# Kernel tuning notes

Measured on AMD Instinct MI355X. Metric: run time of the kernel, lower is better.

## Reference

```python
import jax, jax.numpy as jnp
import numpy as np

B, T, F, H, FC1, NC = 16384, 56, 56, 20, 128, 2


def setup_inputs() -> dict:
    key = jax.random.key(0)
    ks = jax.random.split(key, 12)
    s_in = 1.0 / np.sqrt(H)  # PyTorch GRU init scale
    d = {
        'x': jax.random.normal(ks[0], (B, T, F), jnp.float32),
        'W_ih0': jax.random.uniform(ks[1], (3 * H, F), jnp.float32, -s_in, s_in),
        'W_hh0': jax.random.uniform(ks[2], (3 * H, H), jnp.float32, -s_in, s_in),
        'b_ih0': jax.random.uniform(ks[3], (3 * H,), jnp.float32, -s_in, s_in),
        'b_hh0': jax.random.uniform(ks[4], (3 * H,), jnp.float32, -s_in, s_in),
        'W_ih1': jax.random.uniform(ks[5], (3 * H, H), jnp.float32, -s_in, s_in),
        'W_hh1': jax.random.uniform(ks[6], (3 * H, H), jnp.float32, -s_in, s_in),
        'b_ih1': jax.random.uniform(ks[7], (3 * H,), jnp.float32, -s_in, s_in),
        'b_hh1': jax.random.uniform(ks[8], (3 * H,), jnp.float32, -s_in, s_in),
        'W_fc1': jax.random.uniform(ks[9], (FC1, T * H), jnp.float32, -1 / np.sqrt(T * H), 1 / np.sqrt(T * H)),
        'b_fc1': jnp.zeros((FC1,), jnp.float32),
        'W_fc2': jax.random.uniform(ks[10], (NC, FC1), jnp.float32, -1 / np.sqrt(FC1), 1 / np.sqrt(FC1)),
        'b_fc2': jnp.zeros((NC,), jnp.float32),
    }
    return d


def gru_layer(x, W_ih, W_hh, b_ih, b_hh):
    # x: [B, T, Fin] -> output [B, T, H]; PyTorch gate order: r, z, n
    xproj = jnp.einsum('bti,gi->btg', x, W_ih) + b_ih  # [B, T, 3H]

    def step(h, xp):
        gh = h @ W_hh.T + b_hh
        i_r, i_z, i_n = jnp.split(xp, 3, axis=-1)
        h_r, h_z, h_n = jnp.split(gh, 3, axis=-1)
        r = jax.nn.sigmoid(i_r + h_r)
        z = jax.nn.sigmoid(i_z + h_z)
        n = jnp.tanh(i_n + r * h_n)
        h_new = (1.0 - z) * n + z * h
        return h_new, h_new

    h0 = jnp.zeros((x.shape[0], W_hh.shape[1]), x.dtype)
    _, ys = jax.lax.scan(step, h0, jnp.swapaxes(xproj, 0, 1))  # [T, B, H]
    return jnp.swapaxes(ys, 0, 1)


def reference(x, W_ih0, W_hh0, b_ih0, b_hh0, W_ih1, W_hh1, b_ih1, b_hh1,
              W_fc1, b_fc1, W_fc2, b_fc2):
    h1 = gru_layer(x, W_ih0, W_hh0, b_ih0, b_hh0)   # [B, T, H]
    h2 = gru_layer(h1, W_ih1, W_hh1, b_ih1, b_hh1)  # [B, T, H]
    flat = h2.reshape(h2.shape[0], -1)              # [B, T*H]
    y = flat @ W_fc1.T + b_fc1
    y = y @ W_fc2.T + b_fc2
    return y
```

## Files before the change

### kernel.cpp

```cpp
#include <hip/hip_runtime.h>


#define Bsz  16384
#define Tt   56
#define Ff   56
#define Hh   20
#define Gg   60
#define FC1n 128
#define THn  1120
#define BT   (Bsz * Tt)

#define WS_WEFF 0
#define WS_BEFF 2240
#define WS_WT   2242
#define WS_XP   5632
#define WS_NEED_BYTES ((size_t)(WS_XP + (size_t)BT * Gg) * 4)

typedef __attribute__((address_space(1))) const unsigned char gas_uchar;
typedef __attribute__((address_space(3))) unsigned char las_uchar;
typedef __attribute__((ext_vector_type(2))) float f32x2;

__device__ __forceinline__ float rdlane(float v, int l) {
  return __uint_as_float(__builtin_amdgcn_readlane(__float_as_uint(v), l));
}
__device__ __forceinline__ float bperm(int addr, float v) {
  return __uint_as_float(__builtin_amdgcn_ds_bpermute(addr, __float_as_uint(v)));
}
__device__ __forceinline__ float fast_rcp(float x) { return __builtin_amdgcn_rcpf(x); }
__device__ __forceinline__ float sigmoid_fast(float x) { return fast_rcp(1.0f + __expf(-x)); }
__device__ __forceinline__ float tanh_fast(float x) { return 1.0f - 2.0f * fast_rcp(1.0f + __expf(2.0f * x)); }

__device__ __forceinline__ f32x2 mk2(float a, float b) { f32x2 r; r.x = a; r.y = b; return r; }

__device__ __forceinline__ f32x2 pkfma_s(f32x2 hs, f32x2 wv, f32x2 c) {
  f32x2 d;
  asm("v_pk_fma_f32 %0, %1, %2, %3" : "=v"(d) : "s"(hs), "v"(wv), "v"(c));
  return d;
}
__device__ __forceinline__ f32x2 pkfma_v(f32x2 a, f32x2 b, f32x2 c) {
  f32x2 d;
  asm("v_pk_fma_f32 %0, %1, %2, %3" : "=v"(d) : "v"(a), "v"(b), "v"(c));
  return d;
}
__device__ __forceinline__ f32x2 pkfma_w(f32x2 xx, f32x2 w, f32x2 c) {
  f32x2 d;
  asm("v_pk_fma_f32 %0, %1, %2, %3" : "=v"(d) : "v"(xx), "s"(w), "v"(c));
  return d;
}
__device__ __forceinline__ f32x2 pkadd(f32x2 a, f32x2 b) {
  f32x2 d;
  asm("v_pk_add_f32 %0, %1, %2" : "=v"(d) : "v"(a), "v"(b));
  return d;
}

__device__ __forceinline__ void gru_cell(float xg, float hg, int addrR, int addrZ, float& hm) {
  float sg = sigmoid_fast(xg + hg);
  float rr = bperm(addrR, sg);
  float nn = tanh_fast(fmaf(rr, hg, xg));
  float zz = bperm(addrZ, sg);
  hm = fmaf(zz, hm - nn, nn);
}

__global__ void prep_all(const float* __restrict__ Wfc1, const float* __restrict__ bfc1,
                         const float* __restrict__ Wfc2, const float* __restrict__ bfc2,
                         const float* __restrict__ Wih0, float* __restrict__ ws) {
  int i = blockIdx.x * blockDim.x + threadIdx.x;
  if (i < THn) {
    float s0a = 0.f, s1a = 0.f, s0b = 0.f, s1b = 0.f;
    float s0c = 0.f, s1c = 0.f, s0d = 0.f, s1d = 0.f;
#pragma unroll 4
    for (int j = 0; j < FC1n; j += 4) {
      float wa = Wfc1[(j + 0) * THn + i];
      float wb = Wfc1[(j + 1) * THn + i];
      float wc = Wfc1[(j + 2) * THn + i];
      float wd = Wfc1[(j + 3) * THn + i];
      s0a = fmaf(wa, Wfc2[j + 0], s0a); s1a = fmaf(wa, Wfc2[FC1n + j + 0], s1a);
      s0b = fmaf(wb, Wfc2[j + 1], s0b); s1b = fmaf(wb, Wfc2[FC1n + j + 1], s1b);
      s0c = fmaf(wc, Wfc2[j + 2], s0c); s1c = fmaf(wc, Wfc2[FC1n + j + 2], s1c);
      s0d = fmaf(wd, Wfc2[j + 3], s0d); s1d = fmaf(wd, Wfc2[FC1n + j + 3], s1d);
    }
    ws[WS_WEFF + i * 2 + 0] = (s0a + s0b) + (s0c + s0d);
    ws[WS_WEFF + i * 2 + 1] = (s1a + s1b) + (s1c + s1d);
  } else if (i < THn + 2) {
    int c = i - THn;
    float s = bfc2[c];
    for (int j = 0; j < FC1n; ++j) s = fmaf(bfc1[j], Wfc2[c * FC1n + j], s);
    ws[WS_BEFF + c] = s;
  } else if (i < THn + 2 + Ff * Gg) {
    int j = i - (THn + 2);
    int f = j / 60;
    int rem = j % 60;
    int p = rem >> 1, c = rem & 1;
    ws[WS_WT + j] = Wih0[(2 * p + c) * Ff + f];
  }
}

#define PadW 57
__global__ __launch_bounds__(256, 2) void xproj_kernel(
    const float* __restrict__ x, const float* __restrict__ bih0,
    const float* __restrict__ wschunk , float* __restrict__ xp) {
  __shared__ float xs[256 * PadW];
  const int tid = threadIdx.x;
  const size_t blk0 = (size_t)blockIdx.x * 256;

  const float4* xg = (const float4*)(x + blk0 * Ff);
#pragma unroll
  for (int i = 0; i < 14; ++i) {
    int p = i * 256 + tid;
    float4 v = xg[p];
    int r = p / 14, c = p % 14;
    *(float4*)&xs[r * PadW + c * 4] = v;
  }
  __syncthreads();

  f32x2 acc2[30];
  const f32x2* b2 = (const f32x2*)bih0;
#pragma unroll
  for (int p = 0; p < 30; ++p) acc2[p] = b2[p];

  const f32x2* wt2 = (const f32x2*)wschunk;
#pragma unroll 1
  for (int f4 = 0; f4 < 14; ++f4) {
    float4 xv = *(const float4*)&xs[tid * PadW + f4 * 4];
    const f32x2* w0 = wt2 + (size_t)(f4 * 4) * 30;
    {
      f32x2 xx = mk2(xv.x, xv.x);
#pragma unroll
      for (int p = 0; p < 30; ++p) acc2[p] = pkfma_w(xx, w0[p], acc2[p]);
    }
    {
      f32x2 xx = mk2(xv.y, xv.y);
      const f32x2* w = w0 + 30;
#pragma unroll
      for (int p = 0; p < 30; ++p) acc2[p] = pkfma_w(xx, w[p], acc2[p]);
    }
    {
      f32x2 xx = mk2(xv.z, xv.z);
      const f32x2* w = w0 + 60;
#pragma unroll
      for (int p = 0; p < 30; ++p) acc2[p] = pkfma_w(xx, w[p], acc2[p]);
    }
    {
      f32x2 xx = mk2(xv.w, xv.w);
      const f32x2* w = w0 + 90;
#pragma unroll
      for (int p = 0; p < 30; ++p) acc2[p] = pkfma_w(xx, w[p], acc2[p]);
    }
  }
  float4* out = (float4*)(xp + (blk0 + tid) * Gg);
#pragma unroll
  for (int q = 0; q < 15; ++q)
    out[q] = make_float4(acc2[2 * q].x, acc2[2 * q].y, acc2[2 * q + 1].x, acc2[2 * q + 1].y);
}

__global__ __launch_bounds__(256, 4) void gru_scan_xp2(
    const float* __restrict__ xp,
    const float* __restrict__ Whh0, const float* __restrict__ bhh0,
    const float* __restrict__ Wih1, const float* __restrict__ bih1,
    const float* __restrict__ Whh1, const float* __restrict__ bhh1,
    const float* __restrict__ ws, float* __restrict__ y) {
  __shared__ float weff[2 * THn + 2];
  __shared__ __align__(16) float hstage[4][2][64];
  for (int idx = threadIdx.x; idx < 2 * THn + 2; idx += 256) weff[idx] = ws[idx];
  __syncthreads();

  const int lane = threadIdx.x & 63;
  const int wv = threadIdx.x >> 6;
  const int b0 = (blockIdx.x * 4 + wv) * 2;
  const int g = (lane < Gg) ? lane : 0;

  f32x2 whh0p[10], wih1p[10], whh1p[10];
#pragma unroll
  for (int i = 0; i < 10; ++i) whh0p[i] = *(const f32x2*)&Whh0[g * Hh + 2 * i];
#pragma unroll
  for (int i = 0; i < 10; ++i) wih1p[i] = *(const f32x2*)&Wih1[g * Hh + 2 * i];
#pragma unroll
  for (int i = 0; i < 10; ++i) whh1p[i] = *(const f32x2*)&Whh1[g * Hh + 2 * i];

  const f32x2 cb0  = mk2(bhh0[g], 0.f);
  const f32x2 cb1i = mk2(bih1[g], 0.f);
  const f32x2 cb1h = mk2(bhh1[g], 0.f);
  const f32x2 zz2  = mk2(0.f, 0.f);

  float hmA[2] = {0.f, 0.f};
  float hmB[2] = {0.f, 0.f};
  f32x2 hA2[2][10];
#pragma unroll
  for (int e = 0; e < 2; ++e)
#pragma unroll
    for (int i = 0; i < 10; ++i) hA2[e][i] = zz2;

  hstage[wv][0][lane] = 0.f;
  hstage[wv][1][lane] = 0.f;

  float ya[2] = {0.f, 0.f};
  float yb[2] = {0.f, 0.f};

  const int addrR = ((lane >= 40) ? (lane - 40) : lane) * 4;
  const int addrZ = ((lane >= 40) ? (lane - 20) : lane) * 4;
  const int jm = (lane >= 40 && lane < Gg) ? lane - 40 : 0;

  const float* xpb = xp + (size_t)b0 * (Tt * Gg);
  int off[2];
  float xc[2], xn[2];
#pragma unroll
  for (int e = 0; e < 2; ++e) { off[e] = e * (Tt * Gg) + g; xc[e] = xpb[off[e]]; }

#pragma unroll 1
  for (int t = 0; t < Tt; ++t) {
    if (t < Tt - 1) {
#pragma unroll
      for (int e = 0; e < 2; ++e) xn[e] = xpb[off[e] + Gg];
    }
#pragma unroll
    for (int e = 0; e < 2; ++e) {
      f32x2 a = pkfma_s(hA2[e][0], whh0p[0], cb0);
      f32x2 b = pkfma_s(hA2[e][1], whh0p[1], zz2);
#pragma unroll
      for (int i = 2; i < 10; i += 2) {
        a = pkfma_s(hA2[e][i], whh0p[i], a);
        b = pkfma_s(hA2[e][i + 1], whh0p[i + 1], b);
      }
      f32x2 s = pkadd(a, b);
      float hg = s.x + s.y;
      gru_cell(xc[e], hg, addrR, addrZ, hmA[e]);
#pragma unroll
      for (int i = 0; i < 10; ++i)
        hA2[e][i] = mk2(rdlane(hmA[e], 40 + 2 * i), rdlane(hmA[e], 41 + 2 * i));
    }
#pragma unroll
    for (int e = 0; e < 2; ++e) {
      f32x2 ai = pkfma_s(hA2[e][0], wih1p[0], cb1i);
      f32x2 bi = pkfma_s(hA2[e][1], wih1p[1], zz2);
#pragma unroll
      for (int i = 2; i < 10; i += 2) {
        ai = pkfma_s(hA2[e][i], wih1p[i], ai);
        bi = pkfma_s(hA2[e][i + 1], wih1p[i + 1], bi);
      }
      const float4* hb = (const float4*)&hstage[wv][e][40];
      float4 q0 = hb[0], q1 = hb[1], q2 = hb[2], q3 = hb[3], q4 = hb[4];
      f32x2 ah = pkfma_v(mk2(q0.x, q0.y), whh1p[0], cb1h);
      f32x2 bh = pkfma_v(mk2(q0.z, q0.w), whh1p[1], zz2);
      ah = pkfma_v(mk2(q1.x, q1.y), whh1p[2], ah);
      bh = pkfma_v(mk2(q1.z, q1.w), whh1p[3], bh);
      ah = pkfma_v(mk2(q2.x, q2.y), whh1p[4], ah);
      bh = pkfma_v(mk2(q2.z, q2.w), whh1p[5], bh);
      ah = pkfma_v(mk2(q3.x, q3.y), whh1p[6], ah);
      bh = pkfma_v(mk2(q3.z, q3.w), whh1p[7], bh);
      ah = pkfma_v(mk2(q4.x, q4.y), whh1p[8], ah);
      bh = pkfma_v(mk2(q4.z, q4.w), whh1p[9], bh);
      f32x2 si = pkadd(ai, bi);
      float ig = si.x + si.y;
      f32x2 sh = pkadd(ah, bh);
      float hg = sh.x + sh.y;
      gru_cell(ig, hg, addrR, addrZ, hmB[e]);
      hstage[wv][e][lane] = hmB[e];
    }
    {
      float2 wv2 = *(const float2*)&weff[(t * Hh + jm) * 2];
#pragma unroll
      for (int e = 0; e < 2; ++e) {
        ya[e] = fmaf(hmB[e], wv2.x, ya[e]);
        yb[e] = fmaf(hmB[e], wv2.y, yb[e]);
      }
    }
#pragma unroll
    for (int e = 0; e < 2; ++e) { xc[e] = xn[e]; off[e] += Gg; }
  }

  const bool active = (lane >= 40 && lane < Gg);
#pragma unroll
  for (int e = 0; e < 2; ++e) {
    if (!active) { ya[e] = 0.f; yb[e] = 0.f; }
  }
#pragma unroll
  for (int off2 = 32; off2 >= 1; off2 >>= 1) {
#pragma unroll
    for (int e = 0; e < 2; ++e) {
      ya[e] += __shfl_xor(ya[e], off2, 64);
      yb[e] += __shfl_xor(yb[e], off2, 64);
    }
  }
  if (lane == 0) {
    float be0 = weff[WS_BEFF], be1 = weff[WS_BEFF + 1];
    float4 o0 = make_float4(ya[0] + be0, yb[0] + be1, ya[1] + be0, yb[1] + be1);
    *(float4*)(y + (size_t)b0 * 2) = o0;
  }
}

__global__ __launch_bounds__(256) void gru_scan_fb(
    const float* __restrict__ x,
    const float* __restrict__ Wih0, const float* __restrict__ Whh0,
    const float* __restrict__ bih0, const float* __restrict__ bhh0,
    const float* __restrict__ Wih1, const float* __restrict__ Whh1,
    const float* __restrict__ bih1, const float* __restrict__ bhh1,
    const float* __restrict__ ws, float* __restrict__ y) {
  __shared__ float weff[2 * THn];
  __shared__ __align__(16) float xstage[4][2][Ff];
  for (int idx = threadIdx.x; idx < 2 * THn; idx += 256) weff[idx] = ws[idx];
  __syncthreads();

  const int lane = threadIdx.x & 63;
  const int wv = threadIdx.x >> 6;
  const int b = blockIdx.x * 4 + wv;
  const int g = (lane < Gg) ? lane : 0;

  float wih0[Ff], whh0[Hh], wih1[Hh], whh1[Hh];
#pragma unroll
  for (int f = 0; f < Ff; ++f) wih0[f] = Wih0[g * Ff + f];
#pragma unroll
  for (int k = 0; k < Hh; ++k) whh0[k] = Whh0[g * Hh + k];
#pragma unroll
  for (int k = 0; k < Hh; ++k) wih1[k] = Wih1[g * Hh + k];
#pragma unroll
  for (int k = 0; k < Hh; ++k) whh1[k] = Whh1[g * Hh + k];
  const float bi0 = bih0[g], bh0 = bhh0[g], bi1 = bih1[g], bh1 = bhh1[g];

  float sA[Hh], sB[Hh];
#pragma unroll
  for (int k = 0; k < Hh; ++k) { sA[k] = 0.f; sB[k] = 0.f; }
  float hmA = 0.f, hmB = 0.f, y0 = 0.f, y1 = 0.f;

  const float* xrow = x + (size_t)b * (Tt * Ff);
  const int addrR = ((lane >= 40) ? (lane - 40) : lane) * 4;
  const int addrZ = ((lane >= 40) ? (lane - 20) : lane) * 4;
  const int jm = (lane >= 40 && lane < Gg) ? lane - 40 : 0;

  if (lane < 14) {
    __builtin_amdgcn_global_load_lds((gas_uchar*)(xrow + lane * 4),
                                     (las_uchar*)&xstage[wv][0][0], 16, 0, 0);
  }

#pragma unroll 1
  for (int t = 0; t < Tt; ++t) {
    const float* nxt = xrow + ((t < Tt - 1) ? Ff : 0);
    if (lane < 14) {
      __builtin_amdgcn_global_load_lds((gas_uchar*)(nxt + lane * 4),
                                       (las_uchar*)&xstage[wv][(t + 1) & 1][0], 16, 0, 0);
    }
    asm volatile("s_waitcnt vmcnt(1)" ::: "memory");
    const float4* xs = (const float4*)&xstage[wv][t & 1][0];
    {
      float a0 = bi0, a1 = 0.f, a2 = 0.f, a3 = 0.f;
#pragma unroll
      for (int i = 0; i < 14; ++i) {
        float4 xv = xs[i];
        a0 = fmaf(xv.x, wih0[4 * i + 0], a0);
        a1 = fmaf(xv.y, wih0[4 * i + 1], a1);
        a2 = fmaf(xv.z, wih0[4 * i + 2], a2);
        a3 = fmaf(xv.w, wih0[4 * i + 3], a3);
      }
      float ig = (a0 + a1) + (a2 + a3);
      float h0 = bh0, h1v = 0.f;
#pragma unroll
      for (int k = 0; k < Hh; k += 2) {
        h0 = fmaf(sA[k + 0], whh0[k + 0], h0);
        h1v = fmaf(sA[k + 1], whh0[k + 1], h1v);
      }
      float hg = h0 + h1v;
      gru_cell(ig, hg, addrR, addrZ, hmA);
#pragma unroll
      for (int j = 0; j < Hh; ++j) sA[j] = rdlane(hmA, 40 + j);
    }
    {
      float a0 = bi1, a1 = 0.f;
#pragma unroll
      for (int k = 0; k < Hh; k += 2) {
        a0 = fmaf(sA[k + 0], wih1[k + 0], a0);
        a1 = fmaf(sA[k + 1], wih1[k + 1], a1);
      }
      float ig = a0 + a1;
      float h0 = bh1, h1v = 0.f;
#pragma unroll
      for (int k = 0; k < Hh; k += 2) {
        h0 = fmaf(sB[k + 0], whh1[k + 0], h0);
        h1v = fmaf(sB[k + 1], whh1[k + 1], h1v);
      }
      float hg = h0 + h1v;
      gru_cell(ig, hg, addrR, addrZ, hmB);
#pragma unroll
      for (int j = 0; j < Hh; ++j) sB[j] = rdlane(hmB, 40 + j);
    }
    {
      float2 wv2 = *(const float2*)&weff[(t * Hh + jm) * 2];
      y0 = fmaf(hmB, wv2.x, y0);
      y1 = fmaf(hmB, wv2.y, y1);
    }
    xrow += Ff;
  }

  if (!(lane >= 40 && lane < Gg)) { y0 = 0.f; y1 = 0.f; }
#pragma unroll
  for (int off = 32; off >= 1; off >>= 1) {
    y0 += __shfl_xor(y0, off, 64);
    y1 += __shfl_xor(y1, off, 64);
  }
  if (lane == 0) {
    float be0 = ws[WS_BEFF + 0], be1 = ws[WS_BEFF + 1];
    float2 out = make_float2(y0 + be0, y1 + be1);
    *(float2*)(y + (size_t)b * 2) = out;
  }
}

extern "C" void kernel_launch(void* const* d_in, const int* in_sizes, int n_in,
                              void* d_out, int out_size, void* d_ws, size_t ws_size,
                              hipStream_t stream) {
  const float* x    = (const float*)d_in[0];
  const float* Wih0 = (const float*)d_in[1];
  const float* Whh0 = (const float*)d_in[2];
  const float* bih0 = (const float*)d_in[3];
  const float* bhh0 = (const float*)d_in[4];
  const float* Wih1 = (const float*)d_in[5];
  const float* Whh1 = (const float*)d_in[6];
  const float* bih1 = (const float*)d_in[7];
  const float* bhh1 = (const float*)d_in[8];
  const float* Wfc1 = (const float*)d_in[9];
  const float* bfc1 = (const float*)d_in[10];
  const float* Wfc2 = (const float*)d_in[11];
  const float* bfc2 = (const float*)d_in[12];
  float* ws = (float*)d_ws;
  float* y  = (float*)d_out;

  prep_all<<<18, 256, 0, stream>>>(Wfc1, bfc1, Wfc2, bfc2, Wih0, ws);

  if (ws_size >= WS_NEED_BYTES) {
    float* xp = ws + WS_XP;
    xproj_kernel<<<BT / 256, 256, 0, stream>>>(x, bih0, ws + WS_WT, xp);
    gru_scan_xp2<<<Bsz / 8, 256, 0, stream>>>(xp, Whh0, bhh0, Wih1, bih1,
                                              Whh1, bhh1, ws, y);
  } else {
    gru_scan_fb<<<Bsz / 4, 256, 0, stream>>>(x, Wih0, Whh0, bih0, bhh0,
                                             Wih1, Whh1, bih1, bhh1, ws, y);
  }
}
```

Before: 566.6 us.

## Fuse layer-0 input projection into the GRU scan kernel

Drops the separate xproj kernel, which wrote a [B*T, 60] projection buffer to global memory that the scan kernel then read back. Each wave now streams raw x rows for its two batch elements into LDS via double-buffered global_load_lds, and computes the input-gate projection in-loop with packed FMAs against Wih0 weights held in registers. This removes a large global write and read of intermediate data. In exchange it adds per-step serial compute inside the recurrence, raises register pressure (occupancy hint lowered from 4 to 3), and removes the fallback path.

Result: faster. 517.3 us (-8.7%).

```diff
diff --git a/kernel.cpp b/kernel.cpp
--- a/kernel.cpp
+++ b/kernel.cpp
@@ -8,13 +8,9 @@
 #define Gg   60
 #define FC1n 128
 #define THn  1120
-#define BT   (Bsz * Tt)
 
 #define WS_WEFF 0
 #define WS_BEFF 2240
-#define WS_WT   2242
-#define WS_XP   5632
-#define WS_NEED_BYTES ((size_t)(WS_XP + (size_t)BT * Gg) * 4)
 
 typedef __attribute__((address_space(1))) const unsigned char gas_uchar;
 typedef __attribute__((address_space(3))) unsigned char las_uchar;
@@ -40,11 +36,6 @@
 __device__ __forceinline__ f32x2 pkfma_v(f32x2 a, f32x2 b, f32x2 c) {
   f32x2 d;
   asm("v_pk_fma_f32 %0, %1, %2, %3" : "=v"(d) : "v"(a), "v"(b), "v"(c));
-  return d;
-}
-__device__ __forceinline__ f32x2 pkfma_w(f32x2 xx, f32x2 w, f32x2 c) {
-  f32x2 d;
-  asm("v_pk_fma_f32 %0, %1, %2, %3" : "=v"(d) : "v"(xx), "s"(w), "v"(c));
   return d;
 }
 __device__ __forceinline__ f32x2 pkadd(f32x2 a, f32x2 b) {
@@ -63,7 +54,7 @@
 
 __global__ void prep_all(const float* __restrict__ Wfc1, const float* __restrict__ bfc1,
                          const float* __restrict__ Wfc2, const float* __restrict__ bfc2,
-                         const float* __restrict__ Wih0, float* __restrict__ ws) {
+                         float* __restrict__ ws) {
   int i = blockIdx.x * blockDim.x + threadIdx.x;
   if (i < THn) {
     float s0a = 0.f, s1a = 0.f, s0b = 0.f, s1b = 0.f;
@@ -86,80 +77,18 @@
     float s = bfc2[c];
     for (int j = 0; j < FC1n; ++j) s = fmaf(bfc1[j], Wfc2[c * FC1n + j], s);
     ws[WS_BEFF + c] = s;
-  } else if (i < THn + 2 + Ff * Gg) {
-    int j = i - (THn + 2);
-    int f = j / 60;
-    int rem = j % 60;
-    int p = rem >> 1, c = rem & 1;
-    ws[WS_WT + j] = Wih0[(2 * p + c) * Ff + f];
-  }
-}
-
-#define PadW 57
-__global__ __launch_bounds__(256, 2) void xproj_kernel(
-    const float* __restrict__ x, const float* __restrict__ bih0,
-    const float* __restrict__ wschunk , float* __restrict__ xp) {
-  __shared__ float xs[256 * PadW];
-  const int tid = threadIdx.x;
-  const size_t blk0 = (size_t)blockIdx.x * 256;
-
-  const float4* xg = (const float4*)(x + blk0 * Ff);
-#pragma unroll
-  for (int i = 0; i < 14; ++i) {
-    int p = i * 256 + tid;
-    float4 v = xg[p];
-    int r = p / 14, c = p % 14;
-    *(float4*)&xs[r * PadW + c * 4] = v;
-  }
-  __syncthreads();
-
-  f32x2 acc2[30];
-  const f32x2* b2 = (const f32x2*)bih0;
-#pragma unroll
-  for (int p = 0; p < 30; ++p) acc2[p] = b2[p];
-
-  const f32x2* wt2 = (const f32x2*)wschunk;
-#pragma unroll 1
-  for (int f4 = 0; f4 < 14; ++f4) {
-    float4 xv = *(const float4*)&xs[tid * PadW + f4 * 4];
-    const f32x2* w0 = wt2 + (size_t)(f4 * 4) * 30;
-    {
-      f32x2 xx = mk2(xv.x, xv.x);
-#pragma unroll
-      for (int p = 0; p < 30; ++p) acc2[p] = pkfma_w(xx, w0[p], acc2[p]);
-    }
-    {
-      f32x2 xx = mk2(xv.y, xv.y);
-      const f32x2* w = w0 + 30;
-#pragma unroll
-      for (int p = 0; p < 30; ++p) acc2[p] = pkfma_w(xx, w[p], acc2[p]);
-    }
-    {
-      f32x2 xx = mk2(xv.z, xv.z);
-      const f32x2* w = w0 + 60;
-#pragma unroll
-      for (int p = 0; p < 30; ++p) acc2[p] = pkfma_w(xx, w[p], acc2[p]);
-    }
-    {
-      f32x2 xx = mk2(xv.w, xv.w);
-      const f32x2* w = w0 + 90;
-#pragma unroll
-      for (int p = 0; p < 30; ++p) acc2[p] = pkfma_w(xx, w[p], acc2[p]);
-    }
-  }
-  float4* out = (float4*)(xp + (blk0 + tid) * Gg);
-#pragma unroll
-  for (int q = 0; q < 15; ++q)
-    out[q] = make_float4(acc2[2 * q].x, acc2[2 * q].y, acc2[2 * q + 1].x, acc2[2 * q + 1].y);
-}
-
-__global__ __launch_bounds__(256, 4) void gru_scan_xp2(
-    const float* __restrict__ xp,
+  }
+}
+
+__global__ __launch_bounds__(256, 3) void gru_fused(
+    const float* __restrict__ x,
+    const float* __restrict__ Wih0, const float* __restrict__ bih0,
     const float* __restrict__ Whh0, const float* __restrict__ bhh0,
     const float* __restrict__ Wih1, const float* __restrict__ bih1,
     const float* __restrict__ Whh1, const float* __restrict__ bhh1,
     const float* __restrict__ ws, float* __restrict__ y) {
   __shared__ float weff[2 * THn + 2];
+  __shared__ __align__(16) float xstage[4][2][2 * Ff];
   __shared__ __align__(16) float hstage[4][2][64];
   for (int idx = threadIdx.x; idx < 2 * THn + 2; idx += 256) weff[idx] = ws[idx];
   __syncthreads();
@@ -169,7 +98,9 @@
   const int b0 = (blockIdx.x * 4 + wv) * 2;
   const int g = (lane < Gg) ? lane : 0;
 
-  f32x2 whh0p[10], wih1p[10], whh1p[10];
+  f32x2 wih0p[28], whh0p[10], wih1p[10], whh1p[10];
+#pragma unroll
+  for (int i = 0; i < 28; ++i) wih0p[i] = *(const f32x2*)&Wih0[g * Ff + 2 * i];
 #pragma unroll
   for (int i = 0; i < 10; ++i) whh0p[i] = *(const f32x2*)&Whh0[g * Hh + 2 * i];
 #pragma unroll
@@ -177,6 +108,7 @@
 #pragma unroll
   for (int i = 0; i < 10; ++i) whh1p[i] = *(const f32x2*)&Whh1[g * Hh + 2 * i];
 
+  const f32x2 cbi0 = mk2(bih0[g], 0.f);
   const f32x2 cb0  = mk2(bhh0[g], 0.f);
   const f32x2 cb1i = mk2(bih1[g], 0.f);
   const f32x2 cb1h = mk2(bhh1[g], 0.f);
@@ -200,30 +132,47 @@
   const int addrZ = ((lane >= 40) ? (lane - 20) : lane) * 4;
   const int jm = (lane >= 40 && lane < Gg) ? lane - 40 : 0;
 
-  const float* xpb = xp + (size_t)b0 * (Tt * Gg);
-  int off[2];
-  float xc[2], xn[2];
-#pragma unroll
-  for (int e = 0; e < 2; ++e) { off[e] = e * (Tt * Gg) + g; xc[e] = xpb[off[e]]; }
+  const int le = (lane >= 14) ? 1 : 0;
+  const int lc = lane - le * 14;
+  const float* xsrc = x + (size_t)(b0 + le) * (Tt * Ff) + lc * 4;
+
+  if (lane < 28) {
+    __builtin_amdgcn_global_load_lds((gas_uchar*)xsrc,
+                                     (las_uchar*)&xstage[wv][0][0], 16, 0, 0);
+  }
 
 #pragma unroll 1
   for (int t = 0; t < Tt; ++t) {
-    if (t < Tt - 1) {
-#pragma unroll
-      for (int e = 0; e < 2; ++e) xn[e] = xpb[off[e] + Gg];
-    }
+    const float* nxt = xsrc + ((t < Tt - 1) ? Ff : 0);
+    if (lane < 28) {
+      __builtin_amdgcn_global_load_lds((gas_uchar*)nxt,
+                                       (las_uchar*)&xstage[wv][(t + 1) & 1][0], 16, 0, 0);
+    }
+    asm volatile("s_waitcnt vmcnt(1)" ::: "memory");
 #pragma unroll
     for (int e = 0; e < 2; ++e) {
-      f32x2 a = pkfma_s(hA2[e][0], whh0p[0], cb0);
-      f32x2 b = pkfma_s(hA2[e][1], whh0p[1], zz2);
+      const float4* xb = (const float4*)&xstage[wv][t & 1][e * Ff];
+      float4 q = xb[0];
+      f32x2 a = pkfma_v(mk2(q.x, q.y), wih0p[0], cbi0);
+      f32x2 b = pkfma_v(mk2(q.z, q.w), wih0p[1], zz2);
+#pragma unroll
+      for (int i = 1; i < 14; ++i) {
+        q = xb[i];
+        a = pkfma_v(mk2(q.x, q.y), wih0p[2 * i], a);
+        b = pkfma_v(mk2(q.z, q.w), wih0p[2 * i + 1], b);
+      }
+      f32x2 sx = pkadd(a, b);
+      f32x2 c = pkfma_s(hA2[e][0], whh0p[0], cb0);
+      f32x2 d = pkfma_s(hA2[e][1], whh0p[1], zz2);
 #pragma unroll
       for (int i = 2; i < 10; i += 2) {
-        a = pkfma_s(hA2[e][i], whh0p[i], a);
-        b = pkfma_s(hA2[e][i + 1], whh0p[i + 1], b);
-      }
-      f32x2 s = pkadd(a, b);
-      float hg = s.x + s.y;
-      gru_cell(xc[e], hg, addrR, addrZ, hmA[e]);
+        c = pkfma_s(hA2[e][i], whh0p[i], c);
+        d = pkfma_s(hA2[e][i + 1], whh0p[i + 1], d);
+      }
+      f32x2 sh = pkadd(c, d);
+      float xg = sx.x + sx.y;
+      float hg = sh.x + sh.y;
+      gru_cell(xg, hg, addrR, addrZ, hmA[e]);
 #pragma unroll
       for (int i = 0; i < 10; ++i)
         hA2[e][i] = mk2(rdlane(hmA[e], 40 + 2 * i), rdlane(hmA[e], 41 + 2 * i));
@@ -264,8 +213,7 @@
         yb[e] = fmaf(hmB[e], wv2.y, yb[e]);
       }
     }
-#pragma unroll
-    for (int e = 0; e < 2; ++e) { xc[e] = xn[e]; off[e] += Gg; }
+    xsrc += Ff;
   }
 
   const bool active = (lane >= 40 && lane < Gg);
@@ -285,120 +233,6 @@
     float be0 = weff[WS_BEFF], be1 = weff[WS_BEFF + 1];
     float4 o0 = make_float4(ya[0] + be0, yb[0] + be1, ya[1] + be0, yb[1] + be1);
     *(float4*)(y + (size_t)b0 * 2) = o0;
-  }
-}
-
-__global__ __launch_bounds__(256) void gru_scan_fb(
-    const float* __restrict__ x,
-    const float* __restrict__ Wih0, const float* __restrict__ Whh0,
-    const float* __restrict__ bih0, const float* __restrict__ bhh0,
-    const float* __restrict__ Wih1, const float* __restrict__ Whh1,
-    const float* __restrict__ bih1, const float* __restrict__ bhh1,
-    const float* __restrict__ ws, float* __restrict__ y) {
-  __shared__ float weff[2 * THn];
-  __shared__ __align__(16) float xstage[4][2][Ff];
-  for (int idx = threadIdx.x; idx < 2 * THn; idx += 256) weff[idx] = ws[idx];
-  __syncthreads();
-
-  const int lane = threadIdx.x & 63;
-  const int wv = threadIdx.x >> 6;
-  const int b = blockIdx.x * 4 + wv;
-  const int g = (lane < Gg) ? lane : 0;
-
-  float wih0[Ff], whh0[Hh], wih1[Hh], whh1[Hh];
-#pragma unroll
-  for (int f = 0; f < Ff; ++f) wih0[f] = Wih0[g * Ff + f];
-#pragma unroll
-  for (int k = 0; k < Hh; ++k) whh0[k] = Whh0[g * Hh + k];
-#pragma unroll
-  for (int k = 0; k < Hh; ++k) wih1[k] = Wih1[g * Hh + k];
-#pragma unroll
-  for (int k = 0; k < Hh; ++k) whh1[k] = Whh1[g * Hh + k];
-  const float bi0 = bih0[g], bh0 = bhh0[g], bi1 = bih1[g], bh1 = bhh1[g];
-
-  float sA[Hh], sB[Hh];
-#pragma unroll
-  for (int k = 0; k < Hh; ++k) { sA[k] = 0.f; sB[k] = 0.f; }
-  float hmA = 0.f, hmB = 0.f, y0 = 0.f, y1 = 0.f;
-
-  const float* xrow = x + (size_t)b * (Tt * Ff);
-  const int addrR = ((lane >= 40) ? (lane - 40) : lane) * 4;
-  const int addrZ = ((lane >= 40) ? (lane - 20) : lane) * 4;
-  const int jm = (lane >= 40 && lane < Gg) ? lane - 40 : 0;
-
-  if (lane < 14) {
-    __builtin_amdgcn_global_load_lds((gas_uchar*)(xrow + lane * 4),
-                                     (las_uchar*)&xstage[wv][0][0], 16, 0, 0);
-  }
-
-#pragma unroll 1
-  for (int t = 0; t < Tt; ++t) {
-    const float* nxt = xrow + ((t < Tt - 1) ? Ff : 0);
-    if (lane < 14) {
-      __builtin_amdgcn_global_load_lds((gas_uchar*)(nxt + lane * 4),
-                                       (las_uchar*)&xstage[wv][(t + 1) & 1][0], 16, 0, 0);
-    }
-    asm volatile("s_waitcnt vmcnt(1)" ::: "memory");
-    const float4* xs = (const float4*)&xstage[wv][t & 1][0];
-    {
-      float a0 = bi0, a1 = 0.f, a2 = 0.f, a3 = 0.f;
-#pragma unroll
-      for (int i = 0; i < 14; ++i) {
-        float4 xv = xs[i];
-        a0 = fmaf(xv.x, wih0[4 * i + 0], a0);
-        a1 = fmaf(xv.y, wih0[4 * i + 1], a1);
-        a2 = fmaf(xv.z, wih0[4 * i + 2], a2);
-        a3 = fmaf(xv.w, wih0[4 * i + 3], a3);
-      }
-      float ig = (a0 + a1) + (a2 + a3);
-      float h0 = bh0, h1v = 0.f;
-#pragma unroll
-      for (int k = 0; k < Hh; k += 2) {
-        h0 = fmaf(sA[k + 0], whh0[k + 0], h0);
-        h1v = fmaf(sA[k + 1], whh0[k + 1], h1v);
-      }
-      float hg = h0 + h1v;
-      gru_cell(ig, hg, addrR, addrZ, hmA);
-#pragma unroll
-      for (int j = 0; j < Hh; ++j) sA[j] = rdlane(hmA, 40 + j);
-    }
-    {
-      float a0 = bi1, a1 = 0.f;
-#pragma unroll
-      for (int k = 0; k < Hh; k += 2) {
-        a0 = fmaf(sA[k + 0], wih1[k + 0], a0);
-        a1 = fmaf(sA[k + 1], wih1[k + 1], a1);
-      }
-      float ig = a0 + a1;
-      float h0 = bh1, h1v = 0.f;
-#pragma unroll
-      for (int k = 0; k < Hh; k += 2) {
-        h0 = fmaf(sB[k + 0], whh1[k + 0], h0);
-        h1v = fmaf(sB[k + 1], whh1[k + 1], h1v);
-      }
-      float hg = h0 + h1v;
-      gru_cell(ig, hg, addrR, addrZ, hmB);
-#pragma unroll
-      for (int j = 0; j < Hh; ++j) sB[j] = rdlane(hmB, 40 + j);
-    }
-    {
-      float2 wv2 = *(const float2*)&weff[(t * Hh + jm) * 2];
-      y0 = fmaf(hmB, wv2.x, y0);
-      y1 = fmaf(hmB, wv2.y, y1);
-    }
-    xrow += Ff;
-  }
-
-  if (!(lane >= 40 && lane < Gg)) { y0 = 0.f; y1 = 0.f; }
-#pragma unroll
-  for (int off = 32; off >= 1; off >>= 1) {
-    y0 += __shfl_xor(y0, off, 64);
-    y1 += __shfl_xor(y1, off, 64);
-  }
-  if (lane == 0) {
-    float be0 = ws[WS_BEFF + 0], be1 = ws[WS_BEFF + 1];
-    float2 out = make_float2(y0 + be0, y1 + be1);
-    *(float2*)(y + (size_t)b * 2) = out;
   }
 }
 
@@ -421,15 +255,7 @@
   float* ws = (float*)d_ws;
   float* y  = (float*)d_out;
 
-  prep_all<<<18, 256, 0, stream>>>(Wfc1, bfc1, Wfc2, bfc2, Wih0, ws);
-
-  if (ws_size >= WS_NEED_BYTES) {
-    float* xp = ws + WS_XP;
-    xproj_kernel<<<BT / 256, 256, 0, stream>>>(x, bih0, ws + WS_WT, xp);
-    gru_scan_xp2<<<Bsz / 8, 256, 0, stream>>>(xp, Whh0, bhh0, Wih1, bih1,
-                                              Whh1, bhh1, ws, y);
-  } else {
-    gru_scan_fb<<<Bsz / 4, 256, 0, stream>>>(x, Wih0, Whh0, bih0, bhh0,
-                                             Wih1, Whh1, bih1, bhh1, ws, y);
-  }
-}
+  prep_all<<<5, 256, 0, stream>>>(Wfc1, bfc1, Wfc2, bfc2, ws);
+  gru_fused<<<Bsz / 8, 256, 0, stream>>>(x, Wih0, bih0, Whh0, bhh0,
+                                         Wih1, bih1, Whh1, bhh1, ws, y);
+}
```
